# Kernel optimization log

Measured on AMD Instinct MI355X. Metric: run time of the kernel, lower is better.

Reference implementation:

```python
import jax, jax.numpy as jnp
import numpy as np

N = 50000        # nodes
E = 1_600_000    # edges (avg degree 32)
D_IN = 128
D_H = 128
D_OUT = 128


def expmap0(x):
    # Poincare ball (c=1): expmap0(v) = tanh(||v||) * v / ||v||
    n = jnp.maximum(jnp.linalg.norm(x, axis=-1, keepdims=True), 1e-15)
    return jnp.tanh(n) * x / n


def gat_layer(x, src, dst, W, a_src, a_dst, b, n_nodes):
    # PyG GATConv, heads=1: h = xW; e_ij = LeakyReLU(a_src.h_j + a_dst.h_i);
    # softmax over incoming edges of each target i; out_i = sum_j alpha_ij h_j + b
    h = x @ W                                   # [N, d_out]
    s = h @ a_src                               # [N]
    d = h @ a_dst                               # [N]
    e = jax.nn.leaky_relu(s[src] + d[dst], 0.2)  # [E']
    m = jax.ops.segment_max(e, dst, num_segments=n_nodes)
    num = jnp.exp(e - m[dst])
    den = jax.ops.segment_sum(num, dst, num_segments=n_nodes)
    alpha = num / den[dst]                      # [E']
    out = jax.ops.segment_sum(alpha[:, None] * h[src], dst, num_segments=n_nodes)
    return out + b


def setup_inputs() -> dict:
    key = jax.random.key(0)
    ks = jax.random.split(key, 16)
    p = lambda k, shape: (jax.random.normal(k, shape, jnp.float32) * 0.08)
    inp = {
        "x": jax.random.normal(ks[0], (N, D_IN), jnp.float32),
        "edge_index": jax.random.randint(ks[1], (2, E), 0, N, dtype=jnp.int64)
        if jax.config.jax_enable_x64 else jax.random.randint(ks[1], (2, E), 0, N, dtype=jnp.int32),
        "W1": p(ks[2], (D_IN, D_H)),  "a1s": p(ks[3], (D_H,)), "a1d": p(ks[4], (D_H,)), "b1": jnp.zeros((D_H,), jnp.float32),
        "W2": p(ks[5], (D_H, D_H)),   "a2s": p(ks[6], (D_H,)), "a2d": p(ks[7], (D_H,)), "b2": jnp.zeros((D_H,), jnp.float32),
        "W3": p(ks[8], (D_H, D_OUT)), "a3s": p(ks[9], (D_OUT,)), "a3d": p(ks[10], (D_OUT,)), "b3": jnp.zeros((D_OUT,), jnp.float32),
    }
    return inp


def reference(x, edge_index, W1, a1s, a1d, b1, W2, a2s, a2d, b2, W3, a3s, a3d, b3):
    # add self loops (PyG GATConv default)
    loop = jnp.arange(N, dtype=edge_index.dtype)
    src = jnp.concatenate([edge_index[0], loop])
    dst = jnp.concatenate([edge_index[1], loop])
    h = expmap0(x)
    h = jnp.tanh(gat_layer(h, src, dst, W1, a1s, a1d, b1, N)) * 2
    # dropout(p=0.2) is identity in eval mode
    h = jnp.tanh(gat_layer(h, src, dst, W2, a2s, a2d, b2, N)) * 2
    return gat_layer(h, src, dst, W3, a3s, a3d, b3, N)
```

## Files before the change

### kernel.cpp

```cpp
#include <hip/hip_runtime.h>
#include <math.h>

#define D 128
#define CAP 80
#define CNTS 16

typedef __attribute__((ext_vector_type(8))) short short8;
typedef __attribute__((ext_vector_type(4))) float float4v;
typedef __attribute__((ext_vector_type(4))) _Float16 half4v;
typedef __attribute__((ext_vector_type(4))) int int4v;

__device__ __forceinline__ unsigned short f2bf(float x) {
    unsigned u = __float_as_uint(x);
    u += ((u >> 16) & 1u) + 0x7fffu;
    return (unsigned short)(u >> 16);
}
__device__ __forceinline__ float bf2f(unsigned short h) {
    return __uint_as_float((unsigned)h << 16);
}


__global__ void k_prep(const float* __restrict__ W0, const float* __restrict__ W1,
                       const float* __restrict__ W2, unsigned short* __restrict__ whi,
                       unsigned short* __restrict__ wlo, int* __restrict__ cnt, int N) {
    int id = blockIdx.x * blockDim.x + threadIdx.x;
    if (id < 6144) {
        int l = id >> 11;
        int id2 = id & 2047;
        const float* W = (l == 0) ? W0 : (l == 1) ? W1 : W2;
        int lane = id2 & 63;
        int tile = id2 >> 6;
        int kt = tile & 3;
        int ct = tile >> 2;
        int k0 = kt * 32 + (lane >> 4) * 8;
        int n  = ct * 16 + (lane & 15);
        size_t base = (size_t)l * 16384 + (size_t)id2 * 8;
        for (int j = 0; j < 8; j++) {
            float w = W[(k0 + j) * D + n];
            unsigned short h = f2bf(w);
            whi[base + j] = h;
            wlo[base + j] = f2bf(w - bf2f(h));
        }
    } else {
        int i = id - 6144;
        if (i < N * CNTS) cnt[i] = 0;
    }
}


__global__ __launch_bounds__(256) void k_fill(const int* __restrict__ ei, int E, int N,
                                              int* __restrict__ cnt,
                                              int* __restrict__ bucket) {
    int part = blockIdx.x & 7;
    int slice = blockIdx.x >> 3;
    int nsl = gridDim.x >> 3;
    int lo = (int)((long long)N * part >> 3);
    int hi = (int)((long long)N * (part + 1) >> 3);
    const int4v* dst4 = (const int4v*)(ei + E);
    int nv = E >> 2;
    for (int i = slice * blockDim.x + threadIdx.x; i < nv; i += nsl * blockDim.x) {
        int4v d4 = __builtin_nontemporal_load(&dst4[i]);
        int base = i << 2;
        if (d4.x >= lo && d4.x < hi) {
            int s_ = __builtin_nontemporal_load(&ei[base + 0]);
            int p = atomicAdd(&cnt[d4.x << 4], 1);
            if (p < CAP) bucket[(size_t)d4.x * CAP + p] = s_;
        }
        if (d4.y >= lo && d4.y < hi) {
            int s_ = __builtin_nontemporal_load(&ei[base + 1]);
            int p = atomicAdd(&cnt[d4.y << 4], 1);
            if (p < CAP) bucket[(size_t)d4.y * CAP + p] = s_;
        }
        if (d4.z >= lo && d4.z < hi) {
            int s_ = __builtin_nontemporal_load(&ei[base + 2]);
            int p = atomicAdd(&cnt[d4.z << 4], 1);
            if (p < CAP) bucket[(size_t)d4.z * CAP + p] = s_;
        }
        if (d4.w >= lo && d4.w < hi) {
            int s_ = __builtin_nontemporal_load(&ei[base + 3]);
            int p = atomicAdd(&cnt[d4.w << 4], 1);
            if (p < CAP) bucket[(size_t)d4.w * CAP + p] = s_;
        }
    }
    int tail = E & 3;
    if (slice == 0 && (int)threadIdx.x < tail) {
        int e = (nv << 2) + threadIdx.x;
        int d_ = (ei + E)[e];
        if (d_ >= lo && d_ < hi) {
            int s_ = ei[e];
            int p = atomicAdd(&cnt[d_ << 4], 1);
            if (p < CAP) bucket[(size_t)d_ * CAP + p] = s_;
        }
    }
}


template <bool EXP>
__device__ __forceinline__ void prep_frags(const float* __restrict__ A, int rg, int N,
                                           int quad, short8* bhi, short8* blo) {
    bool valid = rg < N;
    const float* arow = &A[(size_t)(valid ? rg : 0) * D];
    float af[32];
#pragma unroll
    for (int kt = 0; kt < 4; kt++) {
        int k0 = kt * 32 + quad * 8;
        float4 x0 = valid ? *(const float4*)&arow[k0]     : make_float4(0.f, 0.f, 0.f, 0.f);
        float4 x1 = valid ? *(const float4*)&arow[k0 + 4] : make_float4(0.f, 0.f, 0.f, 0.f);
        af[kt * 8 + 0] = x0.x; af[kt * 8 + 1] = x0.y; af[kt * 8 + 2] = x0.z; af[kt * 8 + 3] = x0.w;
        af[kt * 8 + 4] = x1.x; af[kt * 8 + 5] = x1.y; af[kt * 8 + 6] = x1.z; af[kt * 8 + 7] = x1.w;
    }
    if (EXP) {
        float ss = 0.f;
#pragma unroll
        for (int q = 0; q < 32; q++) ss += af[q] * af[q];
        ss += __shfl_xor(ss, 16, 64);
        ss += __shfl_xor(ss, 32, 64);
        float n = fmaxf(sqrtf(ss), 1e-15f);
        float sc = tanhf(n) / n;
#pragma unroll
        for (int q = 0; q < 32; q++) af[q] *= sc;
    }
#pragma unroll
    for (int kt = 0; kt < 4; kt++) {
#pragma unroll
        for (int j = 0; j < 8; j++) {
            float v = af[kt * 8 + j];
            unsigned short h = f2bf(v);
            bhi[kt][j] = (short)h;
            blo[kt][j] = (short)f2bf(v - bf2f(h));
        }
    }
}


template <bool EXP>
__global__ __launch_bounds__(256) void k_gemm(const float* __restrict__ A,
                                              const unsigned short* __restrict__ Whi,
                                              const unsigned short* __restrict__ Wlo,
                                              const float* __restrict__ avS,
                                              const float* __restrict__ avD,
                                              _Float16* __restrict__ H,
                                              float* __restrict__ sA,
                                              float* __restrict__ dA, int N) {
    __shared__ unsigned short WshHi[16384];
    __shared__ unsigned short WshLo[16384];
    int t = threadIdx.x;
    int wv = t >> 6, lane = t & 63, quad = lane >> 4, m = lane & 15;

    {
        const uint4* gh = (const uint4*)Whi;
        const uint4* gl = (const uint4*)Wlo;
        uint4* sh = (uint4*)WshHi;
        uint4* sl = (uint4*)WshLo;
#pragma unroll
        for (int i = 0; i < 8; i++) {
            sh[i * 256 + t] = gh[i * 256 + t];
            sl[i * 256 + t] = gl[i * 256 + t];
        }
    }

    int rg = blockIdx.x * 64 + wv * 16 + m;
    short8 bhi[4], blo[4];
    prep_frags<EXP>(A, rg, N, quad, bhi, blo);

    __syncthreads();

    bool valid = rg < N;

    float4v acc[8];
#pragma unroll
    for (int ct = 0; ct < 8; ct++) acc[ct] = (float4v){0.f, 0.f, 0.f, 0.f};

#pragma unroll
    for (int kt = 0; kt < 4; kt++) {
#pragma unroll
        for (int ct = 0; ct < 8; ct++) {
            int wofs = (((ct << 2) | kt) * 64 + lane) * 8;
            short8 whi = *(const short8*)&WshHi[wofs];
            short8 wlo = *(const short8*)&WshLo[wofs];
            acc[ct] = __builtin_amdgcn_mfma_f32_16x16x32_bf16(wlo, blo[kt], acc[ct], 0, 0, 0);
            acc[ct] = __builtin_amdgcn_mfma_f32_16x16x32_bf16(whi, blo[kt], acc[ct], 0, 0, 0);
            acc[ct] = __builtin_amdgcn_mfma_f32_16x16x32_bf16(wlo, bhi[kt], acc[ct], 0, 0, 0);
            acc[ct] = __builtin_amdgcn_mfma_f32_16x16x32_bf16(whi, bhi[kt], acc[ct], 0, 0, 0);
        }
    }

    if (valid) {
#pragma unroll
        for (int ct = 0; ct < 8; ct++) {
            half4v o;
            o[0] = (_Float16)acc[ct][0];
            o[1] = (_Float16)acc[ct][1];
            o[2] = (_Float16)acc[ct][2];
            o[3] = (_Float16)acc[ct][3];
            *(half4v*)&H[(size_t)rg * D + ct * 16 + quad * 4] = o;
        }
    }

    float ps = 0.f, pd = 0.f;
#pragma unroll
    for (int ct = 0; ct < 8; ct++) {
        int fb = ct * 16 + quad * 4;
        float4 as4 = *(const float4*)&avS[fb];
        float4 ad4 = *(const float4*)&avD[fb];
        ps += acc[ct][0] * as4.x + acc[ct][1] * as4.y + acc[ct][2] * as4.z + acc[ct][3] * as4.w;
        pd += acc[ct][0] * ad4.x + acc[ct][1] * ad4.y + acc[ct][2] * ad4.z + acc[ct][3] * ad4.w;
    }
    ps += __shfl_xor(ps, 16, 64);
    ps += __shfl_xor(ps, 32, 64);
    pd += __shfl_xor(pd, 16, 64);
    pd += __shfl_xor(pd, 32, 64);
    if (quad == 0 && valid) {
        sA[rg] = ps;
        dA[rg] = pd;
    }
}


template <bool ACT>
__global__ __launch_bounds__(256) void k_agg(const _Float16* __restrict__ H,
                                             const float* __restrict__ sA,
                                             const float* __restrict__ dA,
                                             const int* __restrict__ cnt,
                                             const int* __restrict__ bucket,
                                             const float* __restrict__ bias,
                                             float* __restrict__ out, int N) {
    int lane = threadIdx.x & 63;
    int node = blockIdx.x * 4 + (threadIdx.x >> 6);
    if (node >= N) return;
    int deg   = __builtin_amdgcn_readfirstlane(cnt[node << 4]);
    if (deg > CAP) deg = CAP;
    int start = node * CAP;
    int end   = start + deg;
    const int* csr = bucket;
    const half4v* Hv = (const half4v*)H;
    float di  = dA[node];
    int half  = lane >> 5;
    int hq    = lane & 31;
    int cq    = hq * 4;

    float ax = 0.f, ay = 0.f, az = 0.f, aw = 0.f;
    float den = 0.f;
    int j = start;

    for (; j + 8 <= end; j += 8) {
        int s0 = csr[j + 0], s1 = csr[j + 1], s2 = csr[j + 2], s3 = csr[j + 3];
        int s4 = csr[j + 4], s5 = csr[j + 5], s6 = csr[j + 6], s7 = csr[j + 7];
        float e0 = sA[s0] + di, e1 = sA[s1] + di, e2 = sA[s2] + di, e3 = sA[s3] + di;
        float e4 = sA[s4] + di, e5 = sA[s5] + di, e6 = sA[s6] + di, e7 = sA[s7] + di;
        e0 = (e0 > 0.f) ? e0 : 0.2f * e0;
        e1 = (e1 > 0.f) ? e1 : 0.2f * e1;
        e2 = (e2 > 0.f) ? e2 : 0.2f * e2;
        e3 = (e3 > 0.f) ? e3 : 0.2f * e3;
        e4 = (e4 > 0.f) ? e4 : 0.2f * e4;
        e5 = (e5 > 0.f) ? e5 : 0.2f * e5;
        e6 = (e6 > 0.f) ? e6 : 0.2f * e6;
        e7 = (e7 > 0.f) ? e7 : 0.2f * e7;
        float p0 = __expf(e0), p1 = __expf(e1), p2 = __expf(e2), p3 = __expf(e3);
        float p4 = __expf(e4), p5 = __expf(e5), p6 = __expf(e6), p7 = __expf(e7);
        int   ra = half ? s1 : s0;
        int   rb = half ? s3 : s2;
        int   rc = half ? s5 : s4;
        int   rd = half ? s7 : s6;
        float wa = half ? p1 : p0;
        float wb = half ? p3 : p2;
        float wc = half ? p5 : p4;
        float wd = half ? p7 : p6;
        half4v ha = Hv[(size_t)ra * 32 + hq];
        half4v hb = Hv[(size_t)rb * 32 + hq];
        half4v hc = Hv[(size_t)rc * 32 + hq];
        half4v hd = Hv[(size_t)rd * 32 + hq];
        den += (wa + wb) + (wc + wd);
        ax += wa * (float)ha[0] + wb * (float)hb[0] + wc * (float)hc[0] + wd * (float)hd[0];
        ay += wa * (float)ha[1] + wb * (float)hb[1] + wc * (float)hc[1] + wd * (float)hd[1];
        az += wa * (float)ha[2] + wb * (float)hb[2] + wc * (float)hc[2] + wd * (float)hd[2];
        aw += wa * (float)ha[3] + wb * (float)hb[3] + wc * (float)hc[3] + wd * (float)hd[3];
    }
    if (j + 4 <= end) {
        int s0 = csr[j + 0], s1 = csr[j + 1], s2 = csr[j + 2], s3 = csr[j + 3];
        float e0 = sA[s0] + di, e1 = sA[s1] + di, e2 = sA[s2] + di, e3 = sA[s3] + di;
        e0 = (e0 > 0.f) ? e0 : 0.2f * e0;
        e1 = (e1 > 0.f) ? e1 : 0.2f * e1;
        e2 = (e2 > 0.f) ? e2 : 0.2f * e2;
        e3 = (e3 > 0.f) ? e3 : 0.2f * e3;
        float p0 = __expf(e0), p1 = __expf(e1), p2 = __expf(e2), p3 = __expf(e3);
        int   ra = half ? s1 : s0;
        int   rb = half ? s3 : s2;
        float wa = half ? p1 : p0;
        float wb = half ? p3 : p2;
        half4v ha = Hv[(size_t)ra * 32 + hq];
        half4v hb = Hv[(size_t)rb * 32 + hq];
        den += wa + wb;
        ax += wa * (float)ha[0] + wb * (float)hb[0];
        ay += wa * (float)ha[1] + wb * (float)hb[1];
        az += wa * (float)ha[2] + wb * (float)hb[2];
        aw += wa * (float)ha[3] + wb * (float)hb[3];
        j += 4;
    }
    if (j + 2 <= end) {
        int s0 = csr[j + 0], s1 = csr[j + 1];
        float e0 = sA[s0] + di, e1 = sA[s1] + di;
        e0 = (e0 > 0.f) ? e0 : 0.2f * e0;
        e1 = (e1 > 0.f) ? e1 : 0.2f * e1;
        float p0 = __expf(e0), p1 = __expf(e1);
        int   ra = half ? s1 : s0;
        float wa = half ? p1 : p0;
        den += wa;
        half4v ha = Hv[(size_t)ra * 32 + hq];
        ax += wa * (float)ha[0]; ay += wa * (float)ha[1];
        az += wa * (float)ha[2]; aw += wa * (float)ha[3];
        j += 2;
    }
    if (j < end && half == 0) {
        int s0 = csr[j];
        float e0 = sA[s0] + di;
        e0 = (e0 > 0.f) ? e0 : 0.2f * e0;
        float p0 = __expf(e0);
        den += p0;
        half4v ha = Hv[(size_t)s0 * 32 + hq];
        ax += p0 * (float)ha[0]; ay += p0 * (float)ha[1];
        az += p0 * (float)ha[2]; aw += p0 * (float)ha[3];
    }

    if (half == 0) {
        float e0 = sA[node] + di;
        e0 = (e0 > 0.f) ? e0 : 0.2f * e0;
        float p0 = __expf(e0);
        den += p0;
        half4v ha = Hv[(size_t)node * 32 + hq];
        ax += p0 * (float)ha[0]; ay += p0 * (float)ha[1];
        az += p0 * (float)ha[2]; aw += p0 * (float)ha[3];
    }

    ax  += __shfl_xor(ax, 32, 64);
    ay  += __shfl_xor(ay, 32, 64);
    az  += __shfl_xor(az, 32, 64);
    aw  += __shfl_xor(aw, 32, 64);
    den += __shfl_xor(den, 32, 64);

    if (half == 0) {
        float iv = 1.f / den;
        float4 b4 = *(const float4*)&bias[cq];
        float vx = ax * iv + b4.x;
        float vy = ay * iv + b4.y;
        float vz = az * iv + b4.z;
        float vw = aw * iv + b4.w;
        if (ACT) {
            vx = 2.f * tanhf(vx);
            vy = 2.f * tanhf(vy);
            vz = 2.f * tanhf(vz);
            vw = 2.f * tanhf(vw);
        }
        *(float4*)&out[(size_t)node * D + cq] = make_float4(vx, vy, vz, vw);
    }
}


extern "C" void kernel_launch(void* const* d_in, const int* in_sizes, int n_in,
                              void* d_out, int out_size, void* d_ws, size_t ws_size,
                              hipStream_t stream) {
    const int N = in_sizes[0] / D;
    const int E = in_sizes[1] / 2;
    const float* x = (const float*)d_in[0];
    const int* ei = (const int*)d_in[1];
    const float* Wm[3] = {(const float*)d_in[2], (const float*)d_in[6], (const float*)d_in[10]};
    const float* aS[3] = {(const float*)d_in[3], (const float*)d_in[7], (const float*)d_in[11]};
    const float* aD[3] = {(const float*)d_in[4], (const float*)d_in[8], (const float*)d_in[12]};
    const float* bb[3] = {(const float*)d_in[5], (const float*)d_in[9], (const float*)d_in[13]};

    char* ws = (char*)d_ws;
    size_t off = 0;
    auto alloc = [&](size_t bytes) -> void* {
        void* p = ws + off;
        off = (off + bytes + 511) & ~(size_t)511;
        return p;
    };
    float*     bufA   = (float*)alloc((size_t)N * D * 4);
    _Float16*  bufB   = (_Float16*)alloc((size_t)N * D * 2);
    float*     sArr   = (float*)alloc((size_t)N * 4);
    float*     dArr   = (float*)alloc((size_t)N * 4);
    int*       cnt    = (int*)alloc((size_t)N * CNTS * 4);
    int*       bucket = (int*)alloc((size_t)N * CAP * 4);
    unsigned short* whiB = (unsigned short*)alloc((size_t)3 * D * D * 2);
    unsigned short* wloB = (unsigned short*)alloc((size_t)3 * D * D * 2);
    (void)ws_size; (void)n_in; (void)out_size;

    k_prep<<<(6144 + N * CNTS + 255) / 256, 256, 0, stream>>>(Wm[0], Wm[1], Wm[2],
                                                              whiB, wloB, cnt, N);
    k_fill<<<2048, 256, 0, stream>>>(ei, E, N, cnt, bucket);

    const int gemmBlocks = (N + 63) / 64;
    for (int l = 0; l < 3; l++) {
        const unsigned short* whi = whiB + (size_t)l * 16384;
        const unsigned short* wlo = wloB + (size_t)l * 16384;
        if (l == 0) {
            k_gemm<true><<<gemmBlocks, 256, 0, stream>>>(x, whi, wlo, aS[0], aD[0],
                                                         bufB, sArr, dArr, N);
        } else {
            k_gemm<false><<<gemmBlocks, 256, 0, stream>>>(bufA, whi, wlo, aS[l], aD[l],
                                                          bufB, sArr, dArr, N);
        }
        if (l < 2) {
            k_agg<true><<<(N + 3) / 4, 256, 0, stream>>>(bufB, sArr, dArr, cnt, bucket,
                                                         bb[l], bufA, N);
        } else {
            k_agg<false><<<(N + 3) / 4, 256, 0, stream>>>(bufB, sArr, dArr, cnt, bucket,
                                                          bb[l], (float*)d_out, N);
        }
    }
}
```

Before: 407.9 us.

## Fuse edge bucket fill with first-layer GEMM into one heterogeneous launch

```diff
diff --git a/kernel.cpp b/kernel.cpp
--- a/kernel.cpp
+++ b/kernel.cpp
@@ -48,17 +48,15 @@
 }
 
 
-__global__ __launch_bounds__(256) void k_fill(const int* __restrict__ ei, int E, int N,
-                                              int* __restrict__ cnt,
-                                              int* __restrict__ bucket) {
-    int part = blockIdx.x & 7;
-    int slice = blockIdx.x >> 3;
-    int nsl = gridDim.x >> 3;
+__device__ __forceinline__ void fill_body(int part, int slice, int nsl,
+                                          const int* __restrict__ ei, int E, int N,
+                                          int* __restrict__ cnt,
+                                          int* __restrict__ bucket) {
     int lo = (int)((long long)N * part >> 3);
     int hi = (int)((long long)N * (part + 1) >> 3);
     const int4v* dst4 = (const int4v*)(ei + E);
     int nv = E >> 2;
-    for (int i = slice * blockDim.x + threadIdx.x; i < nv; i += nsl * blockDim.x) {
+    for (int i = slice * 256 + (int)threadIdx.x; i < nv; i += nsl * 256) {
         int4v d4 = __builtin_nontemporal_load(&dst4[i]);
         int base = i << 2;
         if (d4.x >= lo && d4.x < hi) {
@@ -132,6 +130,88 @@
     }
 }
 
+
+template <bool EXP>
+__device__ __forceinline__ void gemm_body(int bid, const float* __restrict__ A,
+                                          const unsigned short* __restrict__ Whi,
+                                          const unsigned short* __restrict__ Wlo,
+                                          const float* __restrict__ avS,
+                                          const float* __restrict__ avD,
+                                          _Float16* __restrict__ H,
+                                          float* __restrict__ sA,
+                                          float* __restrict__ dA, int N,
+                                          unsigned short* WshHi, unsigned short* WshLo) {
+    int t = threadIdx.x;
+    int wv = t >> 6, lane = t & 63, quad = lane >> 4, m = lane & 15;
+
+    {
+        const uint4* gh = (const uint4*)Whi;
+        const uint4* gl = (const uint4*)Wlo;
+        uint4* sh = (uint4*)WshHi;
+        uint4* sl = (uint4*)WshLo;
+#pragma unroll
+        for (int i = 0; i < 8; i++) {
+            sh[i * 256 + t] = gh[i * 256 + t];
+            sl[i * 256 + t] = gl[i * 256 + t];
+        }
+    }
+
+    int rg = bid * 64 + wv * 16 + m;
+    short8 bhi[4], blo[4];
+    prep_frags<EXP>(A, rg, N, quad, bhi, blo);
+
+    __syncthreads();
+
+    bool valid = rg < N;
+
+    float4v acc[8];
+#pragma unroll
+    for (int ct = 0; ct < 8; ct++) acc[ct] = (float4v){0.f, 0.f, 0.f, 0.f};
+
+#pragma unroll
+    for (int kt = 0; kt < 4; kt++) {
+#pragma unroll
+        for (int ct = 0; ct < 8; ct++) {
+            int wofs = (((ct << 2) | kt) * 64 + lane) * 8;
+            short8 whi = *(const short8*)&WshHi[wofs];
+            short8 wlo = *(const short8*)&WshLo[wofs];
+            acc[ct] = __builtin_amdgcn_mfma_f32_16x16x32_bf16(wlo, blo[kt], acc[ct], 0, 0, 0);
+            acc[ct] = __builtin_amdgcn_mfma_f32_16x16x32_bf16(whi, blo[kt], acc[ct], 0, 0, 0);
+            acc[ct] = __builtin_amdgcn_mfma_f32_16x16x32_bf16(wlo, bhi[kt], acc[ct], 0, 0, 0);
+            acc[ct] = __builtin_amdgcn_mfma_f32_16x16x32_bf16(whi, bhi[kt], acc[ct], 0, 0, 0);
+        }
+    }
+
+    if (valid) {
+#pragma unroll
+        for (int ct = 0; ct < 8; ct++) {
+            half4v o;
+            o[0] = (_Float16)acc[ct][0];
+            o[1] = (_Float16)acc[ct][1];
+            o[2] = (_Float16)acc[ct][2];
+            o[3] = (_Float16)acc[ct][3];
+            *(half4v*)&H[(size_t)rg * D + ct * 16 + quad * 4] = o;
+        }
+    }
+
+    float ps = 0.f, pd = 0.f;
+#pragma unroll
+    for (int ct = 0; ct < 8; ct++) {
+        int fb = ct * 16 + quad * 4;
+        float4 as4 = *(const float4*)&avS[fb];
+        float4 ad4 = *(const float4*)&avD[fb];
+        ps += acc[ct][0] * as4.x + acc[ct][1] * as4.y + acc[ct][2] * as4.z + acc[ct][3] * as4.w;
+        pd += acc[ct][0] * ad4.x + acc[ct][1] * ad4.y + acc[ct][2] * ad4.z + acc[ct][3] * ad4.w;
+    }
+    ps += __shfl_xor(ps, 16, 64);
+    ps += __shfl_xor(ps, 32, 64);
+    pd += __shfl_xor(pd, 16, 64);
+    pd += __shfl_xor(pd, 32, 64);
+    if (quad == 0 && valid) {
+        sA[rg] = ps;
+        dA[rg] = pd;
+    }
+}
 
 template <bool EXP>
 __global__ __launch_bounds__(256) void k_gemm(const float* __restrict__ A,
@@ -144,75 +224,30 @@
                                               float* __restrict__ dA, int N) {
     __shared__ unsigned short WshHi[16384];
     __shared__ unsigned short WshLo[16384];
-    int t = threadIdx.x;
-    int wv = t >> 6, lane = t & 63, quad = lane >> 4, m = lane & 15;
-
-    {
-        const uint4* gh = (const uint4*)Whi;
-        const uint4* gl = (const uint4*)Wlo;
-        uint4* sh = (uint4*)WshHi;
-        uint4* sl = (uint4*)WshLo;
-#pragma unroll
-        for (int i = 0; i < 8; i++) {
-            sh[i * 256 + t] = gh[i * 256 + t];
-            sl[i * 256 + t] = gl[i * 256 + t];
-        }
-    }
-
-    int rg = blockIdx.x * 64 + wv * 16 + m;
-    short8 bhi[4], blo[4];
-    prep_frags<EXP>(A, rg, N, quad, bhi, blo);
-
-    __syncthreads();
-
-    bool valid = rg < N;
-
-    float4v acc[8];
-#pragma unroll
-    for (int ct = 0; ct < 8; ct++) acc[ct] = (float4v){0.f, 0.f, 0.f, 0.f};
-
-#pragma unroll
-    for (int kt = 0; kt < 4; kt++) {
-#pragma unroll
-        for (int ct = 0; ct < 8; ct++) {
-            int wofs = (((ct << 2) | kt) * 64 + lane) * 8;
-            short8 whi = *(const short8*)&WshHi[wofs];
-            short8 wlo = *(const short8*)&WshLo[wofs];
-            acc[ct] = __builtin_amdgcn_mfma_f32_16x16x32_bf16(wlo, blo[kt], acc[ct], 0, 0, 0);
-            acc[ct] = __builtin_amdgcn_mfma_f32_16x16x32_bf16(whi, blo[kt], acc[ct], 0, 0, 0);
-            acc[ct] = __builtin_amdgcn_mfma_f32_16x16x32_bf16(wlo, bhi[kt], acc[ct], 0, 0, 0);
-            acc[ct] = __builtin_amdgcn_mfma_f32_16x16x32_bf16(whi, bhi[kt], acc[ct], 0, 0, 0);
-        }
-    }
-
-    if (valid) {
-#pragma unroll
-        for (int ct = 0; ct < 8; ct++) {
-            half4v o;
-            o[0] = (_Float16)acc[ct][0];
-            o[1] = (_Float16)acc[ct][1];
-            o[2] = (_Float16)acc[ct][2];
-            o[3] = (_Float16)acc[ct][3];
-            *(half4v*)&H[(size_t)rg * D + ct * 16 + quad * 4] = o;
-        }
-    }
-
-    float ps = 0.f, pd = 0.f;
-#pragma unroll
-    for (int ct = 0; ct < 8; ct++) {
-        int fb = ct * 16 + quad * 4;
-        float4 as4 = *(const float4*)&avS[fb];
-        float4 ad4 = *(const float4*)&avD[fb];
-        ps += acc[ct][0] * as4.x + acc[ct][1] * as4.y + acc[ct][2] * as4.z + acc[ct][3] * as4.w;
-        pd += acc[ct][0] * ad4.x + acc[ct][1] * ad4.y + acc[ct][2] * ad4.z + acc[ct][3] * ad4.w;
-    }
-    ps += __shfl_xor(ps, 16, 64);
-    ps += __shfl_xor(ps, 32, 64);
-    pd += __shfl_xor(pd, 16, 64);
-    pd += __shfl_xor(pd, 32, 64);
-    if (quad == 0 && valid) {
-        sA[rg] = ps;
-        dA[rg] = pd;
+    gemm_body<EXP>(blockIdx.x, A, Whi, Wlo, avS, avD, H, sA, dA, N, WshHi, WshLo);
+}
+
+
+__global__ __launch_bounds__(256) void k_gf0(const float* __restrict__ x,
+                                             const unsigned short* __restrict__ Whi,
+                                             const unsigned short* __restrict__ Wlo,
+                                             const float* __restrict__ avS,
+                                             const float* __restrict__ avD,
+                                             _Float16* __restrict__ H,
+                                             float* __restrict__ sA,
+                                             float* __restrict__ dA, int N,
+                                             const int* __restrict__ ei, int E,
+                                             int* __restrict__ cnt,
+                                             int* __restrict__ bucket, int gemmBlocks) {
+    __shared__ unsigned short WshHi[16384];
+    __shared__ unsigned short WshLo[16384];
+    int b = blockIdx.x;
+    if (b < gemmBlocks) {
+        gemm_body<true>(b, x, Whi, Wlo, avS, avD, H, sA, dA, N, WshHi, WshLo);
+    } else {
+        int fb = b - gemmBlocks;
+        int nsl = (gridDim.x - gemmBlocks) >> 3;
+        fill_body(b & 7, fb >> 3, nsl, ei, E, N, cnt, bucket);
     }
 }
 
@@ -387,19 +422,21 @@
 
     k_prep<<<(6144 + N * CNTS + 255) / 256, 256, 0, stream>>>(Wm[0], Wm[1], Wm[2],
                                                               whiB, wloB, cnt, N);
-    k_fill<<<2048, 256, 0, stream>>>(ei, E, N, cnt, bucket);
 
     const int gemmBlocks = (N + 63) / 64;
-    for (int l = 0; l < 3; l++) {
+    const int fillBlocks = 2048;
+
+    k_gf0<<<gemmBlocks + fillBlocks, 256, 0, stream>>>(x, whiB, wloB, aS[0], aD[0],
+                                                       bufB, sArr, dArr, N,
+                                                       ei, E, cnt, bucket, gemmBlocks);
+    k_agg<true><<<(N + 3) / 4, 256, 0, stream>>>(bufB, sArr, dArr, cnt, bucket,
+                                                 bb[0], bufA, N);
+
+    for (int l = 1; l < 3; l++) {
         const unsigned short* whi = whiB + (size_t)l * 16384;
         const unsigned short* wlo = wloB + (size_t)l * 16384;
-        if (l == 0) {
-            k_gemm<true><<<gemmBlocks, 256, 0, stream>>>(x, whi, wlo, aS[0], aD[0],
-                                                         bufB, sArr, dArr, N);
-        } else {
-            k_gemm<false><<<gemmBlocks, 256, 0, stream>>>(bufA, whi, wlo, aS[l], aD[l],
-                                                          bufB, sArr, dArr, N);
-        }
+        k_gemm<false><<<gemmBlocks, 256, 0, stream>>>(bufA, whi, wlo, aS[l], aD[l],
+                                                      bufB, sArr, dArr, N);
         if (l < 2) {
             k_agg<true><<<(N + 3) / 4, 256, 0, stream>>>(bufB, sArr, dArr, cnt, bucket,
                                                          bb[l], bufA, N);
```

New measurement: 466.4 us. +14.3%, slower.
